# Kernel tuning notes

Hardware: AMD Instinct MI355X
Metric: run time of the kernel (lower is better)

The kernel has to match this reference:

```python
import jax, jax.numpy as jnp
import numpy as np

NUM_HEADS = 16
EMBED_DIM = 1024
HEAD_DIM = EMBED_DIM // NUM_HEADS


def setup_inputs() -> dict:
    key = jax.random.key(0)
    ks = jax.random.split(key, 9)
    B, S, D = 4, 2048, EMBED_DIM
    scale = 1.0 / np.sqrt(D)
    inp = {
        "x": jax.random.normal(ks[0], (B, S, D), dtype=jnp.float32),
        "Wq": jax.random.normal(ks[1], (D, D), dtype=jnp.float32) * scale,
        "bq": jnp.zeros((D,), dtype=jnp.float32),
        "Wk": jax.random.normal(ks[2], (D, D), dtype=jnp.float32) * scale,
        "bk": jnp.zeros((D,), dtype=jnp.float32),
        "Wv": jax.random.normal(ks[3], (D, D), dtype=jnp.float32) * scale,
        "bv": jnp.zeros((D,), dtype=jnp.float32),
        "Wo": jax.random.normal(ks[4], (D, D), dtype=jnp.float32) * scale,
        "bo": jnp.zeros((D,), dtype=jnp.float32),
    }
    return inp


def reference(x, Wq, bq, Wk, bk, Wv, bv, Wo, bo):
    # x: [B, S, D]; weights stored torch-style as [out, in] -> use x @ W.T + b
    B, S, D = x.shape
    H, Hd = NUM_HEADS, HEAD_DIM

    def proj(W, b):
        return (jnp.einsum('bsd,ed->bse', x, W) + b).reshape(B, S, H, Hd).transpose(0, 2, 1, 3)

    Q = proj(Wq, bq)  # [B, H, S, Hd]
    K = proj(Wk, bk)
    V = proj(Wv, bv)

    scores = jnp.einsum('bhqd,bhkd->bhqk', Q, K) / jnp.sqrt(jnp.float32(Hd))
    attn = jax.nn.softmax(scores, axis=-1)  # dropout is identity in eval mode
    context = jnp.einsum('bhqk,bhkd->bhqd', attn, V)
    context = context.transpose(0, 2, 1, 3).reshape(B, S, D)
    out = jnp.einsum('bsd,ed->bse', context, Wo) + bo
    return out
```

## Files before the change

### kernel.cpp

```cpp
#include <hip/hip_runtime.h>


#define LOG2E 1.4426950408889634f
#define QSCALE (0.125f * LOG2E)

typedef __bf16 bf16x8 __attribute__((ext_vector_type(8)));
typedef float f32x4 __attribute__((ext_vector_type(4)));
typedef unsigned short u16x4 __attribute__((ext_vector_type(4)));
typedef unsigned short u16x8 __attribute__((ext_vector_type(8)));
typedef unsigned int u32x2 __attribute__((ext_vector_type(2)));

__device__ __forceinline__ unsigned short f2bf(float f) {
  unsigned int u = __builtin_bit_cast(unsigned int, f);
  u += 0x7fffu + ((u >> 16) & 1u);
  return (unsigned short)(u >> 16);
}

__device__ __forceinline__ unsigned int pack2bf(float a, float b) {
  unsigned int ua = __builtin_bit_cast(unsigned int, a);
  unsigned int ub = __builtin_bit_cast(unsigned int, b);
  ua += 0x7fffu + ((ua >> 16) & 1u);
  ub += 0x7fffu + ((ub >> 16) & 1u);
  return __builtin_amdgcn_perm(ub, ua, 0x07060302u);
}

typedef const __attribute__((address_space(1))) void* gptr_t;
typedef __attribute__((address_space(3))) void* lptr_t;
__device__ __forceinline__ void gload16(const void* g, void* l) {
  __builtin_amdgcn_global_load_lds((gptr_t)g, (lptr_t)l, 16, 0, 0);
}

__global__ __launch_bounds__(256) void k_cvt_x(const float* __restrict__ x,
                                               unsigned short* __restrict__ xb) {
  int i = (blockIdx.x * 256 + threadIdx.x) * 4;
  f32x4 v = *(const f32x4*)(x + i);
  u16x4 o; o[0] = f2bf(v[0]); o[1] = f2bf(v[1]); o[2] = f2bf(v[2]); o[3] = f2bf(v[3]);
  *(u16x4*)(xb + i) = o;
}

__global__ __launch_bounds__(256) void k_cvt_w(const float* __restrict__ Wq, const float* __restrict__ Wk,
                                               const float* __restrict__ Wv, const float* __restrict__ Wo,
                                               unsigned short* __restrict__ Wb) {
  int i = (blockIdx.x * 256 + threadIdx.x) * 4;
  int wsel = i >> 20;
  int loc = i & 1048575;
  const float* src = (wsel == 0) ? Wq : (wsel == 1) ? Wk : (wsel == 2) ? Wv : Wo;
  float sc = (wsel == 0) ? QSCALE : 1.0f;
  f32x4 v = *(const f32x4*)(src + loc);
  u16x4 o; o[0] = f2bf(v[0] * sc); o[1] = f2bf(v[1] * sc); o[2] = f2bf(v[2] * sc); o[3] = f2bf(v[3] * sc);
  *(u16x4*)(Wb + i) = o;
}

__global__ __launch_bounds__(256, 2) void k_gemm_qkv(
    const unsigned short* __restrict__ xb, const unsigned short* __restrict__ Wb,
    const float* __restrict__ bq, const float* __restrict__ bk, const float* __restrict__ bv,
    unsigned short* __restrict__ Qb, unsigned short* __restrict__ Kb, unsigned short* __restrict__ Vtb) {
  __shared__ unsigned short As[128 * 32];
  __shared__ unsigned short Bs[128 * 32];
  const int tid = threadIdx.x;
  const int lane = tid & 63;
  const int w = tid >> 6;
  const int wm = w & 1;
  const int wn = w >> 1;
  const int z = blockIdx.z;
  const int m0 = blockIdx.y * 128;
  const int n0 = blockIdx.x * 128;
  const unsigned short* W = Wb + ((size_t)z << 20);

  const int srow = tid >> 2;
  const int sch = (tid & 3) << 3;
  const size_t a0 = (size_t)(m0 + srow) * 1024 + sch;
  const size_t b0 = (size_t)(n0 + srow) * 1024 + sch;

  f32x4 zero4 = {0.f, 0.f, 0.f, 0.f};
  f32x4 acc[4][4];
#pragma unroll
  for (int i = 0; i < 4; ++i)
#pragma unroll
    for (int jj = 0; jj < 4; ++jj) acc[i][jj] = zero4;

  const int fr = lane & 15;
  const int fk = (lane >> 4) << 3;

  for (int kt = 0; kt < 32; ++kt) {
    const int ko = kt << 5;
    __syncthreads();
    gload16(xb + a0 + ko, As + tid * 8);
    gload16(xb + a0 + (size_t)65536 + ko, As + 2048 + tid * 8);
    gload16(W + b0 + ko, Bs + tid * 8);
    gload16(W + b0 + (size_t)65536 + ko, Bs + 2048 + tid * 8);
    __syncthreads();
    bf16x8 af[4], bfr[4];
#pragma unroll
    for (int mt = 0; mt < 4; ++mt)
      af[mt] = *(const bf16x8*)&As[(wm * 64 + mt * 16 + fr) * 32 + fk];
#pragma unroll
    for (int nt = 0; nt < 4; ++nt)
      bfr[nt] = *(const bf16x8*)&Bs[(wn * 64 + nt * 16 + fr) * 32 + fk];
#pragma unroll
    for (int mt = 0; mt < 4; ++mt)
#pragma unroll
      for (int nt = 0; nt < 4; ++nt)
        acc[mt][nt] = __builtin_amdgcn_mfma_f32_16x16x32_bf16(af[mt], bfr[nt], acc[mt][nt], 0, 0, 0);
  }

  const float* bias = (z == 0) ? bq : (z == 1) ? bk : bv;
  const float bsc = (z == 0) ? QSCALE : 1.0f;
  const int rg = (lane >> 4) << 2;
#pragma unroll
  for (int mt = 0; mt < 4; ++mt) {
    const int mb = m0 + wm * 64 + mt * 16 + rg;
    const int b = mb >> 11;
    const int s = mb & 2047;
#pragma unroll
    for (int nt = 0; nt < 4; ++nt) {
      const int n = n0 + wn * 64 + nt * 16 + fr;
      const float bvv = bias[n] * bsc;
      const int h = n >> 6;
      const int d = n & 63;
      if (z == 2) {
        u16x4 pk;
#pragma unroll
        for (int r = 0; r < 4; ++r) pk[r] = f2bf(acc[mt][nt][r] + bvv);
        *(u16x4*)&Vtb[(((size_t)(b * 16 + h) << 6) + d) * 2048 + s] = pk;
      } else {
        unsigned short* O = (z == 0) ? Qb : Kb;
#pragma unroll
        for (int r = 0; r < 4; ++r)
          O[(((size_t)(b * 16 + h) << 11) + s + r) * 64 + d] = f2bf(acc[mt][nt][r] + bvv);
      }
    }
  }
}

__global__ __launch_bounds__(256, 2) void k_flash(
    const unsigned short* __restrict__ Qb, const unsigned short* __restrict__ Kb,
    const unsigned short* __restrict__ Vtb, unsigned short* __restrict__ Ctx) {
  __shared__ unsigned short Ks[128 * 64];
  __shared__ unsigned short Vts[64 * 128];
  __shared__ unsigned short Ps[128 * 128];
  const int tid = threadIdx.x;
  const int lane = tid & 63;
  const int wq = tid >> 6;
  const int fr = lane & 15;
  const int qd = lane >> 4;
  const int bh = blockIdx.y;
  const int q0 = blockIdx.x << 7;
  const size_t hoff = (size_t)bh << 17;
  const unsigned short* Qh = Qb + hoff + ((size_t)q0 << 6);
  const unsigned short* Kh = Kb + hoff;
  const unsigned short* Vh = Vtb + hoff;

  bf16x8 qf[2][2];
#pragma unroll
  for (int qt = 0; qt < 2; ++qt)
#pragma unroll
    for (int ds = 0; ds < 2; ++ds)
      qf[qt][ds] = *(const bf16x8*)&Qh[(wq * 32 + qt * 16 + fr) * 64 + ds * 32 + qd * 8];

  f32x4 zero4 = {0.f, 0.f, 0.f, 0.f};
  f32x4 o_acc[2][4];
  float l_p[2] = {0.f, 0.f};
#pragma unroll
  for (int mt = 0; mt < 2; ++mt)
#pragma unroll
    for (int dt = 0; dt < 4; ++dt) o_acc[mt][dt] = zero4;

  const int prow = wq * 32;

  for (int j = 0; j < 16; ++j) {
    const int k0 = j << 7;
    __syncthreads();
#pragma unroll
    for (int p = 0; p < 4; ++p) {
      int slot = p * 256 + tid;
      int kr = slot >> 3;
      int ch = slot & 7;
      gload16(Kh + (size_t)(k0 + kr) * 64 + ((ch ^ (kr & 7)) << 3), Ks + slot * 8);
    }
#pragma unroll
    for (int p = 0; p < 4; ++p) {
      int slot = p * 256 + tid;
      int dr = slot >> 4;
      int ch = slot & 15;
      gload16(Vh + (size_t)dr * 2048 + k0 + ((ch ^ (dr & 15)) << 3), Vts + slot * 8);
    }
    __syncthreads();

    f32x4 st[2][8];
#pragma unroll
    for (int qt = 0; qt < 2; ++qt)
#pragma unroll
      for (int kt = 0; kt < 8; ++kt) st[qt][kt] = zero4;
#pragma unroll
    for (int kt = 0; kt < 8; ++kt) {
#pragma unroll
      for (int ds = 0; ds < 2; ++ds) {
        int key = kt * 16 + fr;
        int c = ds * 4 + qd;
        bf16x8 kf = *(const bf16x8*)&Ks[key * 64 + ((c ^ (key & 7)) << 3)];
#pragma unroll
        for (int qt = 0; qt < 2; ++qt)
          st[qt][kt] = __builtin_amdgcn_mfma_f32_16x16x32_bf16(kf, qf[qt][ds], st[qt][kt], 0, 0, 0);
      }
    }

#pragma unroll
    for (int qt = 0; qt < 2; ++qt) {
      float ps0 = 0.f, ps1 = 0.f;
#pragma unroll
      for (int kt = 0; kt < 8; ++kt) {
#pragma unroll
        for (int r = 0; r < 4; ++r) st[qt][kt][r] = __builtin_amdgcn_exp2f(st[qt][kt][r]);
        ps0 += st[qt][kt][0] + st[qt][kt][2];
        ps1 += st[qt][kt][1] + st[qt][kt][3];
      }
      l_p[qt] += ps0 + ps1;
    }

#pragma unroll
    for (int qt = 0; qt < 2; ++qt)
#pragma unroll
      for (int kt = 0; kt < 8; ++kt) {
        int row = prow + qt * 16 + fr;
        int c16 = kt * 2 + (qd >> 1);
        int idx = row * 128 + ((c16 ^ (row & 15)) << 3) + (qd & 1) * 4;
        u32x2 pk;
        pk[0] = pack2bf(st[qt][kt][0], st[qt][kt][1]);
        pk[1] = pack2bf(st[qt][kt][2], st[qt][kt][3]);
        *(u32x2*)&Ps[idx] = pk;
      }

#pragma unroll
    for (int ks = 0; ks < 4; ++ks) {
      bf16x8 pf[2];
#pragma unroll
      for (int mt = 0; mt < 2; ++mt) {
        int row = prow + mt * 16 + fr;
        int c16 = ks * 4 + qd;
        pf[mt] = *(const bf16x8*)&Ps[row * 128 + ((c16 ^ (row & 15)) << 3)];
      }
#pragma unroll
      for (int dt = 0; dt < 4; ++dt) {
        int d = dt * 16 + fr;
        int c = ks * 4 + qd;
        bf16x8 vf = *(const bf16x8*)&Vts[d * 128 + ((c ^ (d & 15)) << 3)];
#pragma unroll
        for (int mt = 0; mt < 2; ++mt)
          o_acc[mt][dt] = __builtin_amdgcn_mfma_f32_16x16x32_bf16(pf[mt], vf, o_acc[mt][dt], 0, 0, 0);
      }
    }
  }

  float l_red[2];
#pragma unroll
  for (int mt = 0; mt < 2; ++mt) {
    float lv = l_p[mt];
    lv += __shfl_xor(lv, 16);
    lv += __shfl_xor(lv, 32);
    l_red[mt] = lv;
  }

  const int b = bh >> 4;
  const int h = bh & 15;
#pragma unroll
  for (int mt = 0; mt < 2; ++mt) {
#pragma unroll
    for (int r = 0; r < 4; ++r) {
      float lv = __shfl(l_red[mt], qd * 4 + r);
      float rl = 1.0f / lv;
      int s = q0 + prow + mt * 16 + qd * 4 + r;
      size_t base = (((size_t)b * 2048 + s) << 10) + (h << 6);
#pragma unroll
      for (int dt = 0; dt < 4; ++dt) Ctx[base + dt * 16 + fr] = f2bf(o_acc[mt][dt][r] * rl);
    }
  }
}

__global__ __launch_bounds__(256, 2) void k_gemm_out(
    const unsigned short* __restrict__ Ctx, const unsigned short* __restrict__ Wo,
    const float* __restrict__ bo, float* __restrict__ out) {
  __shared__ unsigned short As[128 * 32];
  __shared__ unsigned short Bs[128 * 32];
  const int tid = threadIdx.x;
  const int lane = tid & 63;
  const int w = tid >> 6;
  const int wm = w & 1;
  const int wn = w >> 1;
  const int m0 = blockIdx.y * 128;
  const int n0 = blockIdx.x * 128;

  const int srow = tid >> 2;
  const int sch = (tid & 3) << 3;
  const size_t a0 = (size_t)(m0 + srow) * 1024 + sch;
  const size_t b0 = (size_t)(n0 + srow) * 1024 + sch;

  f32x4 zero4 = {0.f, 0.f, 0.f, 0.f};
  f32x4 acc[4][4];
#pragma unroll
  for (int i = 0; i < 4; ++i)
#pragma unroll
    for (int jj = 0; jj < 4; ++jj) acc[i][jj] = zero4;

  const int fr = lane & 15;
  const int fk = (lane >> 4) << 3;

  for (int kt = 0; kt < 32; ++kt) {
    const int ko = kt << 5;
    __syncthreads();
    gload16(Ctx + a0 + ko, As + tid * 8);
    gload16(Ctx + a0 + (size_t)65536 + ko, As + 2048 + tid * 8);
    gload16(Wo + b0 + ko, Bs + tid * 8);
    gload16(Wo + b0 + (size_t)65536 + ko, Bs + 2048 + tid * 8);
    __syncthreads();
    bf16x8 af[4], bfr[4];
#pragma unroll
    for (int mt = 0; mt < 4; ++mt)
      af[mt] = *(const bf16x8*)&As[(wm * 64 + mt * 16 + fr) * 32 + fk];
#pragma unroll
    for (int nt = 0; nt < 4; ++nt)
      bfr[nt] = *(const bf16x8*)&Bs[(wn * 64 + nt * 16 + fr) * 32 + fk];
#pragma unroll
    for (int mt = 0; mt < 4; ++mt)
#pragma unroll
      for (int nt = 0; nt < 4; ++nt)
        acc[mt][nt] = __builtin_amdgcn_mfma_f32_16x16x32_bf16(af[mt], bfr[nt], acc[mt][nt], 0, 0, 0);
  }

  const int rg = (lane >> 4) << 2;
#pragma unroll
  for (int mt = 0; mt < 4; ++mt) {
    const int mb = m0 + wm * 64 + mt * 16 + rg;
#pragma unroll
    for (int nt = 0; nt < 4; ++nt) {
      const int n = n0 + wn * 64 + nt * 16 + fr;
      const float bvv = bo[n];
#pragma unroll
      for (int r = 0; r < 4; ++r)
        out[(size_t)(mb + r) * 1024 + n] = acc[mt][nt][r] + bvv;
    }
  }
}

extern "C" void kernel_launch(void* const* d_in, const int* in_sizes, int n_in,
                              void* d_out, int out_size, void* d_ws, size_t ws_size,
                              hipStream_t stream) {
  (void)in_sizes; (void)n_in; (void)out_size; (void)ws_size;
  const float* x = (const float*)d_in[0];
  const float* Wq = (const float*)d_in[1];
  const float* bq = (const float*)d_in[2];
  const float* Wk = (const float*)d_in[3];
  const float* bk = (const float*)d_in[4];
  const float* Wv = (const float*)d_in[5];
  const float* bv = (const float*)d_in[6];
  const float* Wo = (const float*)d_in[7];
  const float* bo = (const float*)d_in[8];
  float* out = (float*)d_out;

  unsigned short* xb = (unsigned short*)d_ws;
  unsigned short* Wb = xb + 8388608;
  unsigned short* Qb = Wb + 4194304;
  unsigned short* Kb = Qb + 8388608;
  unsigned short* Vtb = Kb + 8388608;
  unsigned short* Ctx = xb;

  k_cvt_x<<<8192, 256, 0, stream>>>(x, xb);
  k_cvt_w<<<4096, 256, 0, stream>>>(Wq, Wk, Wv, Wo, Wb);
  k_gemm_qkv<<<dim3(8, 64, 3), 256, 0, stream>>>(xb, Wb, bq, bk, bv, Qb, Kb, Vtb);
  k_flash<<<dim3(16, 64), 256, 0, stream>>>(Qb, Kb, Vtb, Ctx);
  k_gemm_out<<<dim3(8, 64), 256, 0, stream>>>(Ctx, Wb + 3 * 1048576, bo, out);
}
```

Measured before the change: 309.0 us.

## Keep softmax probabilities in registers by permuting V layout, drop P LDS staging

The QKV projection now writes V^T with a permuted sequence order inside each 32-key group. This lets the flash kernel pack the exp'd score accumulators directly into MFMA A-operands in registers instead of round-tripping P through shared memory. Removing the 32KB Ps buffer cuts LDS traffic and LDS footprint, so the launch bound is raised to allow 4 blocks per CU. The risk is register pressure under the tighter occupancy bound and correctness depending on the permutation matching the MFMA fragment layout.

```diff
diff --git a/kernel.cpp b/kernel.cpp
--- a/kernel.cpp
+++ b/kernel.cpp
@@ -8,7 +8,7 @@
 typedef float f32x4 __attribute__((ext_vector_type(4)));
 typedef unsigned short u16x4 __attribute__((ext_vector_type(4)));
 typedef unsigned short u16x8 __attribute__((ext_vector_type(8)));
-typedef unsigned int u32x2 __attribute__((ext_vector_type(2)));
+typedef unsigned int u32x4 __attribute__((ext_vector_type(4)));
 
 __device__ __forceinline__ unsigned short f2bf(float f) {
   unsigned int u = __builtin_bit_cast(unsigned int, f);
@@ -122,7 +122,8 @@
         u16x4 pk;
 #pragma unroll
         for (int r = 0; r < 4; ++r) pk[r] = f2bf(acc[mt][nt][r] + bvv);
-        *(u16x4*)&Vtb[(((size_t)(b * 16 + h) << 6) + d) * 2048 + s] = pk;
+        const int pbase = (s & ~31) | ((s & 12) << 1) | ((s & 16) >> 2);
+        *(u16x4*)&Vtb[(((size_t)(b * 16 + h) << 6) + d) * 2048 + pbase] = pk;
       } else {
         unsigned short* O = (z == 0) ? Qb : Kb;
 #pragma unroll
@@ -133,12 +134,11 @@
   }
 }
 
-__global__ __launch_bounds__(256, 2) void k_flash(
+__global__ __launch_bounds__(256, 4) void k_flash(
     const unsigned short* __restrict__ Qb, const unsigned short* __restrict__ Kb,
     const unsigned short* __restrict__ Vtb, unsigned short* __restrict__ Ctx) {
   __shared__ unsigned short Ks[128 * 64];
   __shared__ unsigned short Vts[64 * 128];
-  __shared__ unsigned short Ps[128 * 128];
   const int tid = threadIdx.x;
   const int lane = tid & 63;
   const int wq = tid >> 6;
@@ -166,8 +166,6 @@
 #pragma unroll
     for (int dt = 0; dt < 4; ++dt) o_acc[mt][dt] = zero4;
 
-  const int prow = wq * 32;
-
   for (int j = 0; j < 16; ++j) {
     const int k0 = j << 7;
     __syncthreads();
@@ -219,26 +217,16 @@
     }
 
 #pragma unroll
-    for (int qt = 0; qt < 2; ++qt)
-#pragma unroll
-      for (int kt = 0; kt < 8; ++kt) {
-        int row = prow + qt * 16 + fr;
-        int c16 = kt * 2 + (qd >> 1);
-        int idx = row * 128 + ((c16 ^ (row & 15)) << 3) + (qd & 1) * 4;
-        u32x2 pk;
-        pk[0] = pack2bf(st[qt][kt][0], st[qt][kt][1]);
-        pk[1] = pack2bf(st[qt][kt][2], st[qt][kt][3]);
-        *(u32x2*)&Ps[idx] = pk;
-      }
-
-#pragma unroll
     for (int ks = 0; ks < 4; ++ks) {
       bf16x8 pf[2];
 #pragma unroll
       for (int mt = 0; mt < 2; ++mt) {
-        int row = prow + mt * 16 + fr;
-        int c16 = ks * 4 + qd;
-        pf[mt] = *(const bf16x8*)&Ps[row * 128 + ((c16 ^ (row & 15)) << 3)];
+        u32x4 pk;
+        pk[0] = pack2bf(st[mt][2 * ks][0], st[mt][2 * ks][1]);
+        pk[1] = pack2bf(st[mt][2 * ks][2], st[mt][2 * ks][3]);
+        pk[2] = pack2bf(st[mt][2 * ks + 1][0], st[mt][2 * ks + 1][1]);
+        pk[3] = pack2bf(st[mt][2 * ks + 1][2], st[mt][2 * ks + 1][3]);
+        pf[mt] = __builtin_bit_cast(bf16x8, pk);
       }
 #pragma unroll
       for (int dt = 0; dt < 4; ++dt) {
@@ -269,7 +257,7 @@
     for (int r = 0; r < 4; ++r) {
       float lv = __shfl(l_red[mt], qd * 4 + r);
       float rl = 1.0f / lv;
-      int s = q0 + prow + mt * 16 + qd * 4 + r;
+      int s = q0 + wq * 32 + mt * 16 + qd * 4 + r;
       size_t base = (((size_t)b * 2048 + s) << 10) + (h << 6);
 #pragma unroll
       for (int dt = 0; dt < 4; ++dt) Ctx[base + dt * 16 + fr] = f2bf(o_acc[mt][dt][r] * rl);
```

New measurement: 413.5 us. 1.34x slower.
